# Optimization experiments

Measured on AMD Instinct MI355X. Metric: run time of the kernel, lower is better.

## Reference

```python
import jax, jax.numpy as jnp
import numpy as np

B_DIM, C_DIM, K_DIM, L_DIM = 16, 64, 207, 64
SUPPORT_LEN, ORDER = 2, 2
C_IN = (ORDER * SUPPORT_LEN + 1) * C_DIM  # 320, include_self=True


def setup_inputs() -> dict:
    key = jax.random.key(0)
    k1, k2, k3, k4 = jax.random.split(key, 4)
    x = jax.random.normal(k1, (B_DIM, C_DIM, K_DIM * L_DIM), dtype=jnp.float32)
    # per-batch adaptive adjacencies (B, K, K), nonnegative like softmax(relu(E1 E2^T))
    a0 = jax.random.uniform(k2, (B_DIM, K_DIM, K_DIM), dtype=jnp.float32)
    a1 = jax.random.uniform(k3, (B_DIM, K_DIM, K_DIM), dtype=jnp.float32)
    # 1x1 conv weight (C_out, C_in) and bias
    W = jax.random.normal(k4, (C_DIM, C_IN), dtype=jnp.float32) * (1.0 / np.sqrt(C_IN))
    b = jnp.zeros((C_DIM,), dtype=jnp.float32)
    return {"x": x, "a0": a0, "a1": a1, "W": W, "b": b, "K": K_DIM, "L": L_DIM}


def reference(x, a0, a1, W, b, K, L):
    B, C = x.shape[0], x.shape[1]
    x = x.reshape(B, C, K, L)  # (B, C, K, L)
    # torch: x1[bl, c, j] = sum_k x[bl, c, k] * a[b, j, k]  (bmm with a^T)
    diffuse = lambda h, a: jnp.einsum('bckl,bjk->bcjl', h, a)
    out = [x]  # include_self=True
    for a in (a0, a1):
        x1 = diffuse(x, a)
        out.append(x1)
        for _ in range(2, ORDER + 1):
            x1 = diffuse(x1, a)
            out.append(x1)
    h = jnp.concatenate(out, axis=1)  # (B, 5C, K, L)
    y = jnp.einsum('bikl,oi->bokl', h, W) + b[None, :, None, None]  # 1x1 conv
    return y.reshape(B, C, K * L)
```

## Files before the change

kernel.cpp:

```cpp
#include <hip/hip_runtime.h>

typedef unsigned short u16;
typedef __bf16 bf16x8 __attribute__((ext_vector_type(8)));
typedef float f32x4 __attribute__((ext_vector_type(4)));

#define NB 16
#define NC 64
#define NK 207
#define NL 64
#define KP 224
#define NKL 13248
#define GROWS 1152
#define CIN 320

__device__ __forceinline__ u16 f2bf(float f) {
  unsigned u = __builtin_bit_cast(unsigned, f);
  u += 0x7FFFu + ((u >> 16) & 1u);
  return (u16)(u >> 16);
}

__device__ __forceinline__ void g2l16(const u16* gsrc, u16* ldst) {
  __builtin_amdgcn_global_load_lds(
      (const __attribute__((address_space(1))) unsigned int*)gsrc,
      (__attribute__((address_space(3))) unsigned int*)ldst, 16, 0, 0);
}

#define XPAD 225

__global__ __launch_bounds__(256) void k_prep_all(
    const float* __restrict__ x, const float* __restrict__ a0,
    const float* __restrict__ a1, const float* __restrict__ W,
    u16* __restrict__ xT, u16* __restrict__ Abf, u16* __restrict__ AbfT,
    u16* __restrict__ G, u16* __restrict__ Wbf) {
  __shared__ float lds[64 * XPAD];
  int id = blockIdx.x, t = threadIdx.x;
  if (id < 1024) {
    int c = id & 63, b = id >> 6;
    const float4* xp4 = (const float4*)(x + (size_t)(b * 64 + c) * NKL);
    for (int i4 = t; i4 < 3312; i4 += 256) {
      float4 v = xp4[i4];
      int k = i4 >> 4, l0 = (i4 & 15) * 4;
      lds[(l0 + 0) * XPAD + k] = v.x;
      lds[(l0 + 1) * XPAD + k] = v.y;
      lds[(l0 + 2) * XPAD + k] = v.z;
      lds[(l0 + 3) * XPAD + k] = v.w;
    }
    __syncthreads();
    for (int ch = t; ch < 64 * 28; ch += 256) {
      int l = ch / 28, kc = ch - l * 28;
      u16 v[8] __attribute__((aligned(16)));
      for (int j = 0; j < 8; j++) {
        int k = kc * 8 + j;
        v[j] = (k < NK) ? f2bf(lds[l * XPAD + k]) : (u16)0;
      }
      *(int4*)(xT + ((size_t)b * 4096 + l * 64 + c) * KP + kc * 8) = *(int4*)v;
    }
  } else if (id < 1280) {
    int local = id - 1024;
    int rt = local & 7, w = (local >> 3) & 1, b = local >> 4;
    const float* A = (w ? a1 : a0) + (size_t)b * NK * NK;
    int m0 = rt * 32;
    for (int idx = t; idx < 32 * 224; idx += 256) {
      int r = idx / 224, k = idx - r * 224;
      int m = m0 + r;
      lds[r * XPAD + k] = (m < NK && k < NK) ? A[m * NK + k] : 0.f;
    }
    __syncthreads();
    for (int ch = t; ch < 32 * 28; ch += 256) {
      int rr = ch / 28, kc = ch - rr * 28;
      u16 v[8] __attribute__((aligned(16)));
      for (int j = 0; j < 8; j++) v[j] = f2bf(lds[rr * XPAD + kc * 8 + j]);
      int m = m0 + rr;
      *(int4*)(Abf + (((size_t)b * 2 + w) * 256 + m) * KP + kc * 8) = *(int4*)v;
      if (m < 208)
        *(int4*)(G + ((size_t)b * GROWS + (1 + 2 * w) * 208 + m) * KP + kc * 8) = *(int4*)v;
    }
    if (rt < 7) {
      for (int ch = t; ch < 224 * 4; ch += 256) {
        int n = ch >> 2, mc = ch & 3;
        u16 v[8] __attribute__((aligned(16)));
        for (int j = 0; j < 8; j++) v[j] = f2bf(lds[(mc * 8 + j) * XPAD + n]);
        *(int4*)(AbfT + (((size_t)b * 2 + w) * 256 + n) * KP + m0 + mc * 8) = *(int4*)v;
      }
    }
  } else if (id < 1312) {
    int local = id - 1280, b = local >> 1, half = local & 1;
    for (int ci = t; ci < 104 * 28; ci += 256) {
      int jr = ci / 28, kc = ci - jr * 28;
      int j = half * 104 + jr;
      u16 v[8] __attribute__((aligned(16)));
      for (int jj = 0; jj < 8; jj++)
        v[jj] = (j == kc * 8 + jj && j < NK) ? (u16)0x3F80 : (u16)0;
      *(int4*)(G + ((size_t)b * GROWS + j) * KP + kc * 8) = *(int4*)v;
    }
  } else if (id < 1328) {
    int b = id - 1312;
    int4 z = {0, 0, 0, 0};
    int4* p = (int4*)(G + (size_t)b * GROWS * KP + (size_t)1040 * KP);
    for (int ci = t; ci < 3136; ci += 256) p[ci] = z;
  } else if (id < 1344) {
    int b = id - 1328;
    int4 z = {0, 0, 0, 0};
    for (int ci = t; ci < 1792; ci += 256) {
      int w = ci / 896, rem = ci - w * 896;
      *(int4*)(AbfT + (((size_t)b * 2 + w) * 256 + 224) * KP + rem * 8) = z;
    }
  } else {
    for (int ci = t; ci < 2560; ci += 256) {
      u16 v[8] __attribute__((aligned(16)));
      for (int j = 0; j < 8; j++) v[j] = f2bf(W[ci * 8 + j]);
      *(int4*)(Wbf + ci * 8) = *(int4*)v;
    }
  }
}

__global__ void k_asq(const u16* __restrict__ Abf, const u16* __restrict__ AbfT,
                      u16* __restrict__ G) {
  int b = blockIdx.z >> 1, w = blockIdx.z & 1;
  int lane = threadIdx.x & 63, wave = threadIdx.x >> 6;
  int wm = wave >> 1, wn = wave & 1;
  const u16* Ab = Abf + ((size_t)b * 2 + w) * 256 * KP;
  const u16* At = AbfT + ((size_t)b * 2 + w) * 256 * KP;
  int m0 = blockIdx.y * 64 + wm * 32;
  int n0 = blockIdx.x * 64 + wn * 32;
  int r = lane & 15, q = lane >> 4;
  f32x4 acc[2][2] = {};
  for (int k0 = 0; k0 < KP; k0 += 32) {
    bf16x8 af[2], bg[2];
    for (int i = 0; i < 2; i++)
      af[i] = *(const bf16x8*)(Ab + (size_t)(m0 + i * 16 + r) * KP + k0 + q * 8);
    for (int i = 0; i < 2; i++)
      bg[i] = *(const bf16x8*)(At + (size_t)(n0 + i * 16 + r) * KP + k0 + q * 8);
    for (int i = 0; i < 2; i++)
      for (int j = 0; j < 2; j++)
        acc[i][j] = __builtin_amdgcn_mfma_f32_16x16x32_bf16(af[i], bg[j], acc[i][j], 0, 0, 0);
  }
  int qblk = 2 + 2 * w;
  for (int i = 0; i < 2; i++)
    for (int j = 0; j < 2; j++)
      for (int rr = 0; rr < 4; rr++) {
        int mj = m0 + i * 16 + q * 4 + rr;
        int nk = n0 + j * 16 + r;
        if (mj < 208 && nk < KP)
          G[((size_t)b * GROWS + qblk * 208 + mj) * KP + nk] = f2bf(acc[i][j][rr]);
      }
}

#define AG 17920
__global__ __launch_bounds__(512, 4) void k_fused(
    const u16* __restrict__ G, const u16* __restrict__ xT,
    const u16* __restrict__ Wbf, const float* __restrict__ bias,
    float* __restrict__ y) {
  __shared__ __align__(16) u16 lds[AG + 2 * 8192];
  int id = blockIdx.x;
  int wg = (id & 7) * 416 + (id >> 3);
  int b = wg / 208, rem = wg % 208;
  int jt = rem >> 4, lt = rem & 15;
  int tid = threadIdx.x, wave = tid >> 6, lane = tid & 63;
  int r = lane & 15, q = lane >> 4;
  const u16* Gb = G + (size_t)b * GROWS * KP;
  const u16* Xb = xT + ((size_t)b * 4096 + lt * 256) * KP;

  for (int i2 = 0; i2 < 5; i2++) {
    int tile = i2 * 8 + wave;
    if (tile < 35) {
      int p = tile / 7, ks = tile - p * 7;
      g2l16(Gb + (size_t)(p * 208 + jt * 16 + r) * KP + ks * 32 + q * 8,
            &lds[tile * 512 + lane * 8]);
    }
  }
  for (int i2 = 0; i2 < 2; i2++) {
    int tile = wave * 2 + i2;
    g2l16(Xb + (size_t)(tile * 16 + r) * KP + q * 8,
          &lds[AG + tile * 512 + lane * 8]);
  }
  asm volatile("s_waitcnt vmcnt(2)" ::: "memory");
  __builtin_amdgcn_s_barrier();

  f32x4 acc1[5][2] = {};
#pragma unroll
  for (int ks = 0; ks < 7; ks++) {
    int cur = ks & 1;
    if (ks < 6) {
      for (int i2 = 0; i2 < 2; i2++) {
        int tile = wave * 2 + i2;
        g2l16(Xb + (size_t)(tile * 16 + r) * KP + (ks + 1) * 32 + q * 8,
              &lds[AG + (cur ^ 1) * 8192 + tile * 512 + lane * 8]);
      }
      asm volatile("s_waitcnt vmcnt(2)" ::: "memory");
    } else {
      asm volatile("s_waitcnt vmcnt(0)" ::: "memory");
    }
    bf16x8 af0 = *(const bf16x8*)&lds[AG + cur * 8192 + (wave * 2 + 0) * 512 + lane * 8];
    bf16x8 af1 = *(const bf16x8*)&lds[AG + cur * 8192 + (wave * 2 + 1) * 512 + lane * 8];
    __builtin_amdgcn_s_setprio(1);
#pragma unroll
    for (int p = 0; p < 5; p++) {
      bf16x8 bg = *(const bf16x8*)&lds[(p * 7 + ks) * 512 + lane * 8];
      acc1[p][0] = __builtin_amdgcn_mfma_f32_16x16x32_bf16(af0, bg, acc1[p][0], 0, 0, 0);
      acc1[p][1] = __builtin_amdgcn_mfma_f32_16x16x32_bf16(af1, bg, acc1[p][1], 0, 0, 0);
    }
    __builtin_amdgcn_s_setprio(0);
  }
  __syncthreads();

#pragma unroll
  for (int p = 0; p < 5; p++)
#pragma unroll
    for (int mf = 0; mf < 2; mf++) {
      int m = (wave * 2 + mf) * 16 + q * 4;
      int t = m >> 6, c = m & 63;
      int cs = c ^ ((r & 7) << 3);
      int idxT = ((p * 16 + r) * 4 + t) * 72 + cs;
      u16 v0 = f2bf(acc1[p][mf][0]), v1 = f2bf(acc1[p][mf][1]);
      u16 v2 = f2bf(acc1[p][mf][2]), v3 = f2bf(acc1[p][mf][3]);
      *(uint2*)&lds[idxT] = make_uint2((unsigned)v0 | ((unsigned)v1 << 16),
                                       (unsigned)v2 | ((unsigned)v3 << 16));
    }
  __syncthreads();

  int mo = wave >> 1, nh = (wave & 1) * 2;
  const u16* Wrow = Wbf + (size_t)(mo * 16 + r) * CIN + q * 8;
  f32x4 acc2[2] = {};
#pragma unroll
  for (int ks = 0; ks < 10; ks++) {
    bf16x8 aw = *(const bf16x8*)(Wrow + ks * 32);
    int p = ks >> 1, c0 = (ks & 1) * 32;
#pragma unroll
    for (int nf = 0; nf < 2; nf++) {
      int n = (nh + nf) * 16 + r;
      int j = n >> 2, t = n & 3;
      int cs = (c0 + q * 8) ^ ((j & 7) << 3);
      bf16x8 bt = *(const bf16x8*)&lds[((p * 16 + j) * 4 + t) * 72 + cs];
      acc2[nf] = __builtin_amdgcn_mfma_f32_16x16x32_bf16(aw, bt, acc2[nf], 0, 0, 0);
    }
  }

  int o0 = mo * 16 + q * 4;
  float4 bv = *(const float4*)&bias[o0];
  float* yb = y + (size_t)b * 64 * NKL;
#pragma unroll
  for (int nf = 0; nf < 2; nf++) {
    int n = (nh + nf) * 16 + r;
    int j = n >> 2, t = n & 3;
    int jnode = jt * 16 + j;
    if (jnode < NK) {
      int col = jnode * 64 + lt * 4 + t;
      yb[(size_t)(o0 + 0) * NKL + col] = acc2[nf][0] + bv.x;
      yb[(size_t)(o0 + 1) * NKL + col] = acc2[nf][1] + bv.y;
      yb[(size_t)(o0 + 2) * NKL + col] = acc2[nf][2] + bv.z;
      yb[(size_t)(o0 + 3) * NKL + col] = acc2[nf][3] + bv.w;
    }
  }
}

extern "C" void kernel_launch(void* const* d_in, const int* in_sizes, int n_in,
                              void* d_out, int out_size, void* d_ws, size_t ws_size,
                              hipStream_t stream) {
  const float* x = (const float*)d_in[0];
  const float* a0 = (const float*)d_in[1];
  const float* a1 = (const float*)d_in[2];
  const float* W = (const float*)d_in[3];
  const float* bias = (const float*)d_in[4];
  float* y = (float*)d_out;
  char* ws = (char*)d_ws;

  size_t off = 0;
  auto alloc = [&](size_t bytes) {
    size_t o = off;
    off = (off + bytes + 511) & ~(size_t)511;
    return o;
  };
  size_t o_xT  = alloc((size_t)NB * 4096 * KP * 2);
  size_t o_G   = alloc((size_t)NB * GROWS * KP * 2);
  size_t o_Ab  = alloc((size_t)NB * 2 * 256 * KP * 2);
  size_t o_At  = alloc((size_t)NB * 2 * 256 * KP * 2);
  size_t o_Wb  = alloc((size_t)64 * CIN * 2);
  (void)ws_size;

  u16* xT  = (u16*)(ws + o_xT);
  u16* G   = (u16*)(ws + o_G);
  u16* Abf = (u16*)(ws + o_Ab);
  u16* AbfT= (u16*)(ws + o_At);
  u16* Wbf = (u16*)(ws + o_Wb);

  k_prep_all<<<dim3(1345), 256, 0, stream>>>(x, a0, a1, W, xT, Abf, AbfT, G, Wbf);
  k_asq<<<dim3(4, 4, 32), 256, 0, stream>>>(Abf, AbfT, G);
  k_fused<<<dim3(16 * 13 * 16), 512, 0, stream>>>(G, xT, Wbf, bias, y);
}
```

Measured before the change: 223.4 us.

## Stream x fragments straight to registers and drop LDS transposes in prep

```diff
diff --git a/kernel.cpp b/kernel.cpp
--- a/kernel.cpp
+++ b/kernel.cpp
@@ -25,66 +25,80 @@
       (__attribute__((address_space(3))) unsigned int*)ldst, 16, 0, 0);
 }
 
-#define XPAD 225
-
-__global__ __launch_bounds__(256) void k_prep_all(
+__global__ __launch_bounds__(256) void k_prep(
     const float* __restrict__ x, const float* __restrict__ a0,
     const float* __restrict__ a1, const float* __restrict__ W,
     u16* __restrict__ xT, u16* __restrict__ Abf, u16* __restrict__ AbfT,
     u16* __restrict__ G, u16* __restrict__ Wbf) {
-  __shared__ float lds[64 * XPAD];
   int id = blockIdx.x, t = threadIdx.x;
   if (id < 1024) {
     int c = id & 63, b = id >> 6;
-    const float4* xp4 = (const float4*)(x + (size_t)(b * 64 + c) * NKL);
-    for (int i4 = t; i4 < 3312; i4 += 256) {
-      float4 v = xp4[i4];
-      int k = i4 >> 4, l0 = (i4 & 15) * 4;
-      lds[(l0 + 0) * XPAD + k] = v.x;
-      lds[(l0 + 1) * XPAD + k] = v.y;
-      lds[(l0 + 2) * XPAD + k] = v.z;
-      lds[(l0 + 3) * XPAD + k] = v.w;
-    }
-    __syncthreads();
-    for (int ch = t; ch < 64 * 28; ch += 256) {
-      int l = ch / 28, kc = ch - l * 28;
-      u16 v[8] __attribute__((aligned(16)));
+    const float* xc = x + (size_t)(b * 64 + c) * NKL;
+    int l = t & 63, kq = t >> 6;
+    u16* drow = xT + ((size_t)b * 4096 + c * 64 + l) * KP;
+#pragma unroll
+    for (int i = 0; i < 7; i++) {
+      int kc = kq * 7 + i;
+      u16 v[8] __attribute__((aligned(16)));
+#pragma unroll
       for (int j = 0; j < 8; j++) {
         int k = kc * 8 + j;
-        v[j] = (k < NK) ? f2bf(lds[l * XPAD + k]) : (u16)0;
-      }
-      *(int4*)(xT + ((size_t)b * 4096 + l * 64 + c) * KP + kc * 8) = *(int4*)v;
-    }
-  } else if (id < 1280) {
+        v[j] = (k < NK) ? f2bf(xc[k * 64 + l]) : (u16)0;
+      }
+      *(int4*)(drow + kc * 8) = *(int4*)v;
+    }
+  } else if (id < 1312) {
     int local = id - 1024;
-    int rt = local & 7, w = (local >> 3) & 1, b = local >> 4;
+    int rt = local % 9, bw = local / 9;
+    int b = bw >> 1, w = bw & 1;
     const float* A = (w ? a1 : a0) + (size_t)b * NK * NK;
-    int m0 = rt * 32;
-    for (int idx = t; idx < 32 * 224; idx += 256) {
-      int r = idx / 224, k = idx - r * 224;
-      int m = m0 + r;
-      lds[r * XPAD + k] = (m < NK && k < NK) ? A[m * NK + k] : 0.f;
-    }
-    __syncthreads();
-    for (int ch = t; ch < 32 * 28; ch += 256) {
-      int rr = ch / 28, kc = ch - rr * 28;
-      u16 v[8] __attribute__((aligned(16)));
-      for (int j = 0; j < 8; j++) v[j] = f2bf(lds[rr * XPAD + kc * 8 + j]);
-      int m = m0 + rr;
-      *(int4*)(Abf + (((size_t)b * 2 + w) * 256 + m) * KP + kc * 8) = *(int4*)v;
-      if (m < 208)
-        *(int4*)(G + ((size_t)b * GROWS + (1 + 2 * w) * 208 + m) * KP + kc * 8) = *(int4*)v;
-    }
-    if (rt < 7) {
-      for (int ch = t; ch < 224 * 4; ch += 256) {
-        int n = ch >> 2, mc = ch & 3;
-        u16 v[8] __attribute__((aligned(16)));
-        for (int j = 0; j < 8; j++) v[j] = f2bf(lds[(mc * 8 + j) * XPAD + n]);
-        *(int4*)(AbfT + (((size_t)b * 2 + w) * 256 + n) * KP + m0 + mc * 8) = *(int4*)v;
-      }
-    }
-  } else if (id < 1312) {
-    int local = id - 1280, b = local >> 1, half = local & 1;
+    u16* Ab = Abf + (size_t)bw * 256 * KP;
+    u16* Gq = G + ((size_t)b * GROWS + (1 + 2 * w) * 208) * KP;
+    if (rt == 8) {
+      int4 z = {0, 0, 0, 0};
+      int4* p = (int4*)(Ab + (size_t)224 * KP);
+      for (int ci = t; ci < 896; ci += 256) p[ci] = z;
+    } else {
+      int m0 = rt * 28;
+      int kc = t & 31, rl = t >> 5;
+      if (kc < 28) {
+#pragma unroll
+        for (int i = 0; i < 4; i++) {
+          int ml = rl + 8 * i;
+          if (ml < 28) {
+            int m = m0 + ml;
+            u16 v[8] __attribute__((aligned(16)));
+#pragma unroll
+            for (int j = 0; j < 8; j++) {
+              int k = kc * 8 + j;
+              v[j] = (m < NK && k < NK) ? f2bf(A[m * NK + k]) : (u16)0;
+            }
+            *(int4*)(Ab + (size_t)m * KP + kc * 8) = *(int4*)v;
+            if (m < 208) *(int4*)(Gq + (size_t)m * KP + kc * 8) = *(int4*)v;
+          }
+        }
+      }
+    }
+  } else if (id < 1536) {
+    int local = id - 1312;
+    int g = local % 7, bw = local / 7;
+    int b = bw >> 1, w = bw & 1;
+    const float* A = (w ? a1 : a0) + (size_t)b * NK * NK;
+    u16* At = AbfT + (size_t)bw * 256 * KP;
+    int n = t;
+#pragma unroll
+    for (int mc4 = 0; mc4 < 4; mc4++) {
+      int mc = g * 4 + mc4;
+      u16 v[8] __attribute__((aligned(16)));
+#pragma unroll
+      for (int j = 0; j < 8; j++) {
+        int m = mc * 8 + j;
+        v[j] = (n < NK && m < NK) ? f2bf(A[m * NK + n]) : (u16)0;
+      }
+      *(int4*)(At + (size_t)n * KP + mc * 8) = *(int4*)v;
+    }
+  } else if (id < 1568) {
+    int local = id - 1536, b = local >> 1, half = local & 1;
     for (int ci = t; ci < 104 * 28; ci += 256) {
       int jr = ci / 28, kc = ci - jr * 28;
       int j = half * 104 + jr;
@@ -92,18 +106,6 @@
       for (int jj = 0; jj < 8; jj++)
         v[jj] = (j == kc * 8 + jj && j < NK) ? (u16)0x3F80 : (u16)0;
       *(int4*)(G + ((size_t)b * GROWS + j) * KP + kc * 8) = *(int4*)v;
-    }
-  } else if (id < 1328) {
-    int b = id - 1312;
-    int4 z = {0, 0, 0, 0};
-    int4* p = (int4*)(G + (size_t)b * GROWS * KP + (size_t)1040 * KP);
-    for (int ci = t; ci < 3136; ci += 256) p[ci] = z;
-  } else if (id < 1344) {
-    int b = id - 1328;
-    int4 z = {0, 0, 0, 0};
-    for (int ci = t; ci < 1792; ci += 256) {
-      int w = ci / 896, rem = ci - w * 896;
-      *(int4*)(AbfT + (((size_t)b * 2 + w) * 256 + 224) * KP + rem * 8) = z;
     }
   } else {
     for (int ci = t; ci < 2560; ci += 256) {
@@ -125,6 +127,7 @@
   int n0 = blockIdx.x * 64 + wn * 32;
   int r = lane & 15, q = lane >> 4;
   f32x4 acc[2][2] = {};
+#pragma unroll
   for (int k0 = 0; k0 < KP; k0 += 32) {
     bf16x8 af[2], bg[2];
     for (int i = 0; i < 2; i++)
@@ -146,12 +149,11 @@
       }
 }
 
-#define AG 17920
-__global__ __launch_bounds__(512, 4) void k_fused(
+__global__ __launch_bounds__(512) void k_fused(
     const u16* __restrict__ G, const u16* __restrict__ xT,
     const u16* __restrict__ Wbf, const float* __restrict__ bias,
     float* __restrict__ y) {
-  __shared__ __align__(16) u16 lds[AG + 2 * 8192];
+  __shared__ __align__(16) u16 lds[23040];
   int id = blockIdx.x;
   int wg = (id & 7) * 416 + (id >> 3);
   int b = wg / 208, rem = wg % 208;
@@ -159,7 +161,6 @@
   int tid = threadIdx.x, wave = tid >> 6, lane = tid & 63;
   int r = lane & 15, q = lane >> 4;
   const u16* Gb = G + (size_t)b * GROWS * KP;
-  const u16* Xb = xT + ((size_t)b * 4096 + lt * 256) * KP;
 
   for (int i2 = 0; i2 < 5; i2++) {
     int tile = i2 * 8 + wave;
@@ -169,38 +170,35 @@
             &lds[tile * 512 + lane * 8]);
     }
   }
-  for (int i2 = 0; i2 < 2; i2++) {
-    int tile = wave * 2 + i2;
-    g2l16(Xb + (size_t)(tile * 16 + r) * KP + q * 8,
-          &lds[AG + tile * 512 + lane * 8]);
-  }
-  asm volatile("s_waitcnt vmcnt(2)" ::: "memory");
+  const u16* arow0;
+  const u16* arow1;
+  {
+    int m0 = (wave * 2 + 0) * 16 + r, m1 = (wave * 2 + 1) * 16 + r;
+    arow0 = xT + ((size_t)b * 4096 + (m0 & 63) * 64 + lt * 4 + (m0 >> 6)) * KP + q * 8;
+    arow1 = xT + ((size_t)b * 4096 + (m1 & 63) * 64 + lt * 4 + (m1 >> 6)) * KP + q * 8;
+  }
+  bf16x8 afA0 = *(const bf16x8*)(arow0);
+  bf16x8 afA1 = *(const bf16x8*)(arow1);
+  asm volatile("s_waitcnt vmcnt(0)" ::: "memory");
   __builtin_amdgcn_s_barrier();
 
   f32x4 acc1[5][2] = {};
 #pragma unroll
   for (int ks = 0; ks < 7; ks++) {
-    int cur = ks & 1;
+    bf16x8 afB0, afB1;
     if (ks < 6) {
-      for (int i2 = 0; i2 < 2; i2++) {
-        int tile = wave * 2 + i2;
-        g2l16(Xb + (size_t)(tile * 16 + r) * KP + (ks + 1) * 32 + q * 8,
-              &lds[AG + (cur ^ 1) * 8192 + tile * 512 + lane * 8]);
-      }
-      asm volatile("s_waitcnt vmcnt(2)" ::: "memory");
-    } else {
-      asm volatile("s_waitcnt vmcnt(0)" ::: "memory");
-    }
-    bf16x8 af0 = *(const bf16x8*)&lds[AG + cur * 8192 + (wave * 2 + 0) * 512 + lane * 8];
-    bf16x8 af1 = *(const bf16x8*)&lds[AG + cur * 8192 + (wave * 2 + 1) * 512 + lane * 8];
+      afB0 = *(const bf16x8*)(arow0 + (ks + 1) * 32);
+      afB1 = *(const bf16x8*)(arow1 + (ks + 1) * 32);
+    }
     __builtin_amdgcn_s_setprio(1);
 #pragma unroll
     for (int p = 0; p < 5; p++) {
       bf16x8 bg = *(const bf16x8*)&lds[(p * 7 + ks) * 512 + lane * 8];
-      acc1[p][0] = __builtin_amdgcn_mfma_f32_16x16x32_bf16(af0, bg, acc1[p][0], 0, 0, 0);
-      acc1[p][1] = __builtin_amdgcn_mfma_f32_16x16x32_bf16(af1, bg, acc1[p][1], 0, 0, 0);
+      acc1[p][0] = __builtin_amdgcn_mfma_f32_16x16x32_bf16(afA0, bg, acc1[p][0], 0, 0, 0);
+      acc1[p][1] = __builtin_amdgcn_mfma_f32_16x16x32_bf16(afA1, bg, acc1[p][1], 0, 0, 0);
     }
     __builtin_amdgcn_s_setprio(0);
+    afA0 = afB0; afA1 = afB1;
   }
   __syncthreads();
 
@@ -209,30 +207,32 @@
 #pragma unroll
     for (int mf = 0; mf < 2; mf++) {
       int m = (wave * 2 + mf) * 16 + q * 4;
-      int t = m >> 6, c = m & 63;
+      int tt = m >> 6, c = m & 63;
       int cs = c ^ ((r & 7) << 3);
-      int idxT = ((p * 16 + r) * 4 + t) * 72 + cs;
+      int idxT = ((p * 16 + r) * 4 + tt) * 72 + cs;
       u16 v0 = f2bf(acc1[p][mf][0]), v1 = f2bf(acc1[p][mf][1]);
       u16 v2 = f2bf(acc1[p][mf][2]), v3 = f2bf(acc1[p][mf][3]);
       *(uint2*)&lds[idxT] = make_uint2((unsigned)v0 | ((unsigned)v1 << 16),
                                        (unsigned)v2 | ((unsigned)v3 << 16));
     }
-  __syncthreads();
-
   int mo = wave >> 1, nh = (wave & 1) * 2;
   const u16* Wrow = Wbf + (size_t)(mo * 16 + r) * CIN + q * 8;
+  bf16x8 aw[10];
+#pragma unroll
+  for (int ks = 0; ks < 10; ks++) aw[ks] = *(const bf16x8*)(Wrow + ks * 32);
+  __syncthreads();
+
   f32x4 acc2[2] = {};
 #pragma unroll
   for (int ks = 0; ks < 10; ks++) {
-    bf16x8 aw = *(const bf16x8*)(Wrow + ks * 32);
     int p = ks >> 1, c0 = (ks & 1) * 32;
 #pragma unroll
     for (int nf = 0; nf < 2; nf++) {
       int n = (nh + nf) * 16 + r;
-      int j = n >> 2, t = n & 3;
+      int j = n >> 2, tt = n & 3;
       int cs = (c0 + q * 8) ^ ((j & 7) << 3);
-      bf16x8 bt = *(const bf16x8*)&lds[((p * 16 + j) * 4 + t) * 72 + cs];
-      acc2[nf] = __builtin_amdgcn_mfma_f32_16x16x32_bf16(aw, bt, acc2[nf], 0, 0, 0);
+      bf16x8 bt = *(const bf16x8*)&lds[((p * 16 + j) * 4 + tt) * 72 + cs];
+      acc2[nf] = __builtin_amdgcn_mfma_f32_16x16x32_bf16(aw[ks], bt, acc2[nf], 0, 0, 0);
     }
   }
 
@@ -242,10 +242,10 @@
 #pragma unroll
   for (int nf = 0; nf < 2; nf++) {
     int n = (nh + nf) * 16 + r;
-    int j = n >> 2, t = n & 3;
+    int j = n >> 2, tt = n & 3;
     int jnode = jt * 16 + j;
     if (jnode < NK) {
-      int col = jnode * 64 + lt * 4 + t;
+      int col = jnode * 64 + lt * 4 + tt;
       yb[(size_t)(o0 + 0) * NKL + col] = acc2[nf][0] + bv.x;
       yb[(size_t)(o0 + 1) * NKL + col] = acc2[nf][1] + bv.y;
       yb[(size_t)(o0 + 2) * NKL + col] = acc2[nf][2] + bv.z;
@@ -284,7 +284,7 @@
   u16* AbfT= (u16*)(ws + o_At);
   u16* Wbf = (u16*)(ws + o_Wb);
 
-  k_prep_all<<<dim3(1345), 256, 0, stream>>>(x, a0, a1, W, xT, Abf, AbfT, G, Wbf);
+  k_prep<<<dim3(1569), 256, 0, stream>>>(x, a0, a1, W, xT, Abf, AbfT, G, Wbf);
   k_asq<<<dim3(4, 4, 32), 256, 0, stream>>>(Abf, AbfT, G);
   k_fused<<<dim3(16 * 13 * 16), 512, 0, stream>>>(G, xT, Wbf, bias, y);
 }
```

New measurement: 271.0 us. 21.3% more time.
